# Kernel tuning notes

Measured on AMD Instinct MI355X. Metric: run time of the kernel, lower is better.

Reference implementation:

```python
import jax, jax.numpy as jnp
import numpy as np

EPS_MSG = 1e-7   # GENConv message eps
EPS_LN = 1e-5    # LayerNorm eps

N, F_IN, D, D_OUT = 32768, 64, 512, 128


def setup_inputs() -> dict:
    key = jax.random.key(0)
    ks = jax.random.split(key, 20)
    s = 0.02
    inp = {
        "batch": jax.random.normal(ks[0], (1, N, F_IN), jnp.float32),
        "W_enc": jax.random.normal(ks[1], (F_IN, D), jnp.float32) * s,
        "b_enc": jnp.zeros((D,), jnp.float32),
        "Wf": jax.random.normal(ks[2], (D, D_OUT), jnp.float32) * s,
        "bf": jnp.zeros((D_OUT,), jnp.float32),
    }
    for l in range(2):
        inp[f"t{l}"] = jnp.array(1.0, jnp.float32)           # learnable softmax temperature
        inp[f"W1_{l}"] = jax.random.normal(ks[3 + 6 * l], (D, 2 * D), jnp.float32) * s
        inp[f"b1_{l}"] = jnp.zeros((2 * D,), jnp.float32)
        inp[f"g_{l}"] = jnp.ones((2 * D,), jnp.float32)      # LN gamma
        inp[f"be_{l}"] = jnp.zeros((2 * D,), jnp.float32)    # LN beta
        inp[f"W2_{l}"] = jax.random.normal(ks[4 + 6 * l], (2 * D, D), jnp.float32) * s
        inp[f"b2_{l}"] = jnp.zeros((D,), jnp.float32)
    return inp


def _layer_norm(z, g, b):
    mu = jnp.mean(z, axis=-1, keepdims=True)
    var = jnp.var(z, axis=-1, keepdims=True)
    return (z - mu) * jax.lax.rsqrt(var + EPS_LN) * g + b


def _deepgcn_layer(x, t, W1, b1, g, be, W2, b2):
    # res+ block: h = conv(act(norm(x))); return x + h   (norm is Identity here)
    h = jax.nn.relu(x)                       # [n, d]
    # GENConv with complete graph: msg_j = relu(h_j) + eps (independent of target i)
    m = jax.nn.relu(h) + EPS_MSG             # [n, d]
    alpha = jax.nn.softmax(t * m, axis=0)    # per-channel softmax over all source nodes
    agg = jnp.sum(alpha * m, axis=0)         # [d]  -- identical for every target node
    out = h + agg[None, :]                   # + x_dst residual inside GENConv
    # GENConv MLP: Linear(d,2d) -> LayerNorm -> ReLU -> Linear(2d,d)
    z = jax.nn.relu(_layer_norm(out @ W1 + b1, g, be))
    out = z @ W2 + b2
    return x + out


def reference(batch, W_enc, b_enc, Wf, bf,
              t0, W1_0, b1_0, g_0, be_0, W2_0, b2_0,
              t1, W1_1, b1_1, g_1, be_1, W2_1, b2_1):
    bsz, n, _ = batch.shape
    x = batch.reshape(bsz * n, -1) @ W_enc + b_enc   # node encoder
    x = _deepgcn_layer(x, t0, W1_0, b1_0, g_0, be_0, W2_0, b2_0)
    x = _deepgcn_layer(x, t1, W1_1, b1_1, g_1, be_1, W2_1, b2_1)
    x = jax.nn.relu(x)                               # layers[0].act(layers[0].norm(x)), norm=Identity
    out = x @ Wf + bf
    return out.reshape(bsz, n, -1)
```

## Files before the change

### kernel.cpp

```cpp
#include <hip/hip_runtime.h>

#define DEV __device__ __forceinline__

typedef __attribute__((ext_vector_type(8))) short s8v;
typedef __attribute__((ext_vector_type(4))) float f4v;

DEV short f2bf(float f) {
  unsigned u = __builtin_bit_cast(unsigned, f);
  u += 0x7fffu + ((u >> 16) & 1u);
  return (short)(u >> 16);
}
DEV float bf2f(short s) {
  unsigned u = ((unsigned)(unsigned short)s) << 16;
  return __builtin_bit_cast(float, u);
}

DEV f4v mfma_16x16x32_bf16(s8v a, s8v b, f4v c) {
  asm("v_mfma_f32_16x16x32_bf16 %0, %1, %2, %0" : "+v"(c) : "v"(a), "v"(b));
  return c;
}

DEV s8v relu8(s8v a) {
#pragma unroll
  for (int i = 0; i < 8; ++i) a[i] = a[i] > (short)0 ? a[i] : (short)0;
  return a;
}

__global__ __launch_bounds__(256) void tconv_k(const float* __restrict__ in,
                                               short* __restrict__ out,
                                               int K, int N) {
  __shared__ float t[64][65];
  const int nb = blockIdx.x * 64, kb = blockIdx.y * 64;
  const int c = threadIdx.x & 63, r0 = threadIdx.x >> 6;
#pragma unroll
  for (int rr = 0; rr < 64; rr += 4)
    t[rr + r0][c] = in[(size_t)(kb + rr + r0) * N + nb + c];
  __syncthreads();
#pragma unroll
  for (int rr = 0; rr < 64; rr += 4)
    out[(size_t)(nb + rr + r0) * K + kb + c] = f2bf(t[c][rr + r0]);
}

__global__ __launch_bounds__(256) void conv_k(const float* __restrict__ in,
                                              short* __restrict__ out, int n4) {
  int i = blockIdx.x * 256 + threadIdx.x;
  if (i >= n4) return;
  float4 v = ((const float4*)in)[i];
  short4 o;
  o.x = f2bf(v.x);
  o.y = f2bf(v.y);
  o.z = f2bf(v.z);
  o.w = f2bf(v.w);
  ((short4*)out)[i] = o;
}

__global__ __launch_bounds__(256) void zero_k(float* p, int n) {
  int i = blockIdx.x * 256 + threadIdx.x;
  if (i < n) p[i] = 0.f;
}

__global__ __launch_bounds__(256) void finalize_k(const float* __restrict__ sums,
                                                  const float* __restrict__ W1,
                                                  const float* __restrict__ b1,
                                                  float* __restrict__ biasEff) {
  __shared__ float agg[512];
  const int tid = threadIdx.x;
  for (int d = tid; d < 512; d += 256) agg[d] = sums[512 + d] / sums[d];
  __syncthreads();
  const int j = blockIdx.x * 256 + tid;
  float a = b1[j];
  for (int d = 0; d < 512; ++d) a += agg[d] * W1[(size_t)d * 1024 + j];
  biasEff[j] = a;
}

__global__ __launch_bounds__(256) void ln_relu_k(short* __restrict__ z,
                                                 const float* __restrict__ g,
                                                 const float* __restrict__ be) {
  const int row = blockIdx.x * 4 + (threadIdx.x >> 6);
  const int lane = threadIdx.x & 63;
  short* zr = z + (size_t)row * 1024;
  s8v c0 = *(const s8v*)&zr[lane * 8];
  s8v c1 = *(const s8v*)&zr[512 + lane * 8];
  float v[16];
  float s = 0.f, q = 0.f;
#pragma unroll
  for (int i = 0; i < 8; ++i) { v[i] = bf2f(c0[i]); v[8 + i] = bf2f(c1[i]); }
#pragma unroll
  for (int i = 0; i < 16; ++i) { s += v[i]; q += v[i] * v[i]; }
#pragma unroll
  for (int o = 32; o > 0; o >>= 1) { s += __shfl_xor(s, o); q += __shfl_xor(q, o); }
  float mu = s * (1.f / 1024.f);
  float var = q * (1.f / 1024.f) - mu * mu;
  float rs = rsqrtf(var + 1e-5f);
  float gv[16], bv[16];
#pragma unroll
  for (int i = 0; i < 8; ++i) {
    gv[i] = g[lane * 8 + i];      gv[8 + i] = g[512 + lane * 8 + i];
    bv[i] = be[lane * 8 + i];     bv[8 + i] = be[512 + lane * 8 + i];
  }
  s8v o0, o1;
#pragma unroll
  for (int i = 0; i < 8; ++i) {
    o0[i] = f2bf(fmaxf((v[i] - mu) * rs * gv[i] + bv[i], 0.f));
    o1[i] = f2bf(fmaxf((v[8 + i] - mu) * rs * gv[8 + i] + bv[8 + i], 0.f));
  }
  *(s8v*)&zr[lane * 8] = o0;
  *(s8v*)&zr[512 + lane * 8] = o1;
}

#define F_ADD   1
#define F_WF32  2
#define F_WBF   4
#define F_SM    8
#define F_RELUA 16

template <int FLAGS>
__global__ __launch_bounds__(256) void gemm_k(const short* __restrict__ A,
                                              const short* __restrict__ Bt,
                                              const float* __restrict__ bias,
                                              const short* __restrict__ Xin,
                                              short* __restrict__ Cb,
                                              float* __restrict__ Cf,
                                              const float* __restrict__ tptr,
                                              float* __restrict__ sums,
                                              int M, int N, int K) {
  __shared__ short lA[128 * 32];
  __shared__ short lB[128 * 32];
  const int tid = threadIdx.x;
  const int lane = tid & 63, wid = tid >> 6;
  const int wr = wid >> 1, wc = wid & 1;
  const int nwg = gridDim.x * gridDim.y;
  const int wg = blockIdx.y * gridDim.x + blockIdx.x;
  const int swz = (wg & 7) * (nwg >> 3) + (wg >> 3);
  const int bx = swz % gridDim.x, by = swz / gridDim.x;
  const int brow = by * 128, bcol = bx * 128;
  const int l15 = lane & 15, lhi = lane >> 4;
  f4v acc[4][4] = {};

  for (int k0 = 0; k0 < K; k0 += 32) {
#pragma unroll
    for (int r = 0; r < 2; ++r) {
      int chunk = r * 256 + wid * 64 + lane;
      int row = chunk >> 2, kc = (chunk & 3) << 3;
      const short* ga = A + (size_t)(brow + row) * K + (k0 + kc);
      const short* gb = Bt + (size_t)(bcol + row) * K + (k0 + kc);
      __builtin_amdgcn_global_load_lds(
          (const __attribute__((address_space(1))) void*)ga,
          (__attribute__((address_space(3))) void*)&lA[(r * 256 + wid * 64) * 8],
          16, 0, 0);
      __builtin_amdgcn_global_load_lds(
          (const __attribute__((address_space(1))) void*)gb,
          (__attribute__((address_space(3))) void*)&lB[(r * 256 + wid * 64) * 8],
          16, 0, 0);
    }
    __syncthreads();
    s8v af[4], bfr[4];
#pragma unroll
    for (int i = 0; i < 4; ++i) {
      af[i]  = *(const s8v*)&lA[(wr * 64 + i * 16 + l15) * 32 + lhi * 8];
      bfr[i] = *(const s8v*)&lB[(wc * 64 + i * 16 + l15) * 32 + lhi * 8];
      if (FLAGS & F_RELUA) af[i] = relu8(af[i]);
    }
#pragma unroll
    for (int mi = 0; mi < 4; ++mi)
#pragma unroll
      for (int ni = 0; ni < 4; ++ni)
        acc[mi][ni] = mfma_16x16x32_bf16(af[mi], bfr[ni], acc[mi][ni]);
    __syncthreads();
  }

  const float tv = (FLAGS & F_SM) ? tptr[0] : 0.f;
  float* sred = (float*)lA;
  if (FLAGS & F_SM) {
    sred[tid] = 0.f;
    __syncthreads();
  }
#pragma unroll
  for (int ni = 0; ni < 4; ++ni) {
    int col = bcol + wc * 64 + ni * 16 + l15;
    float bv = bias[col];
    float se = 0.f, sem = 0.f;
#pragma unroll
    for (int mi = 0; mi < 4; ++mi) {
#pragma unroll
      for (int r = 0; r < 4; ++r) {
        int row = brow + wr * 64 + mi * 16 + lhi * 4 + r;
        size_t idx = (size_t)row * N + col;
        float v = acc[mi][ni][r] + bv;
        if (FLAGS & F_ADD) v += bf2f(Xin[idx]);
        if (FLAGS & F_WF32) Cf[idx] = v;
        if (FLAGS & F_WBF) Cb[idx] = f2bf(v);
        if (FLAGS & F_SM) {
          float m = fmaxf(v, 0.f) + 1e-7f;
          float e = __expf(tv * m);
          se += e;
          sem += e * m;
        }
      }
    }
    if (FLAGS & F_SM) {
      se += __shfl_xor(se, 16);   se += __shfl_xor(se, 32);
      sem += __shfl_xor(sem, 16); sem += __shfl_xor(sem, 32);
      if (lhi == 0) {
        atomicAdd(&sred[wc * 64 + ni * 16 + l15], se);
        atomicAdd(&sred[128 + wc * 64 + ni * 16 + l15], sem);
      }
    }
  }
  if (FLAGS & F_SM) {
    __syncthreads();
    int v = tid >> 7, c = tid & 127;
    atomicAdd(&sums[v * 512 + bcol + c], sred[v * 128 + c]);
  }
}

extern "C" void kernel_launch(void* const* d_in, const int* in_sizes, int n_in,
                              void* d_out, int out_size, void* d_ws,
                              size_t ws_size, hipStream_t stream) {
  (void)in_sizes; (void)n_in; (void)out_size; (void)ws_size;
  const float* batch = (const float*)d_in[0];
  const float* W_enc = (const float*)d_in[1];
  const float* b_enc = (const float*)d_in[2];
  const float* Wf    = (const float*)d_in[3];
  const float* bfv   = (const float*)d_in[4];
  const float* tptr[2] = {(const float*)d_in[5],  (const float*)d_in[12]};
  const float* W1[2]   = {(const float*)d_in[6],  (const float*)d_in[13]};
  const float* b1[2]   = {(const float*)d_in[7],  (const float*)d_in[14]};
  const float* g[2]    = {(const float*)d_in[8],  (const float*)d_in[15]};
  const float* be[2]   = {(const float*)d_in[9],  (const float*)d_in[16]};
  const float* W2[2]   = {(const float*)d_in[10], (const float*)d_in[17]};
  const float* b2[2]   = {(const float*)d_in[11], (const float*)d_in[18]};
  float* out = (float*)d_out;

  const int M = 32768;
  char* ws = (char*)d_ws;
  size_t off = 0;
  auto alloc = [&](size_t bytes) -> char* {
    char* p = ws + off;
    off += (bytes + 255) & ~(size_t)255;
    return p;
  };
  short* xbf    = (short*)alloc((size_t)M * 512 * 2);
  short* zbuf   = (short*)alloc((size_t)M * 1024 * 2);
  short* bbuf   = (short*)alloc((size_t)M * 64 * 2);
  short* wencT  = (short*)alloc(512 * 64 * 2);
  short* w1T0   = (short*)alloc(1024 * 512 * 2);
  short* w2T0   = (short*)alloc(512 * 1024 * 2);
  short* w1T1   = (short*)alloc(1024 * 512 * 2);
  short* w2T1   = (short*)alloc(512 * 1024 * 2);
  short* wfT    = (short*)alloc(128 * 512 * 2);
  float* sums   = (float*)alloc(2 * 1024 * 4);
  float* biasEff= (float*)alloc(1024 * 4);
  short* w1T[2] = {w1T0, w1T1};
  short* w2T[2] = {w2T0, w2T1};

  tconv_k<<<dim3(512 / 64, 64 / 64), 256, 0, stream>>>(W_enc, wencT, 64, 512);
  tconv_k<<<dim3(1024 / 64, 512 / 64), 256, 0, stream>>>(W1[0], w1T[0], 512, 1024);
  tconv_k<<<dim3(512 / 64, 1024 / 64), 256, 0, stream>>>(W2[0], w2T[0], 1024, 512);
  tconv_k<<<dim3(1024 / 64, 512 / 64), 256, 0, stream>>>(W1[1], w1T[1], 512, 1024);
  tconv_k<<<dim3(512 / 64, 1024 / 64), 256, 0, stream>>>(W2[1], w2T[1], 1024, 512);
  tconv_k<<<dim3(128 / 64, 512 / 64), 256, 0, stream>>>(Wf, wfT, 512, 128);

  conv_k<<<(M * 64 / 4 + 255) / 256, 256, 0, stream>>>(batch, bbuf, M * 64 / 4);
  zero_k<<<(2048 + 255) / 256, 256, 0, stream>>>(sums, 2048);

  gemm_k<F_WBF | F_SM><<<dim3(512 / 128, M / 128), 256, 0, stream>>>(
      bbuf, wencT, b_enc, nullptr, xbf, nullptr, tptr[0], sums, M, 512, 64);

  for (int l = 0; l < 2; ++l) {
    finalize_k<<<4, 256, 0, stream>>>(sums + l * 1024, W1[l], b1[l], biasEff);
    gemm_k<F_WBF | F_RELUA><<<dim3(1024 / 128, M / 128), 256, 0, stream>>>(
        xbf, w1T[l], biasEff, nullptr, zbuf, nullptr, nullptr, nullptr,
        M, 1024, 512);
    ln_relu_k<<<M / 4, 256, 0, stream>>>(zbuf, g[l], be[l]);
    if (l == 0) {
      gemm_k<F_ADD | F_WBF | F_SM><<<dim3(512 / 128, M / 128), 256, 0, stream>>>(
          zbuf, w2T[l], b2[l], xbf, xbf, nullptr, tptr[1], sums + 1024,
          M, 512, 1024);
    } else {
      gemm_k<F_ADD | F_WBF><<<dim3(512 / 128, M / 128), 256, 0, stream>>>(
          zbuf, w2T[l], b2[l], xbf, xbf, nullptr, nullptr, nullptr,
          M, 512, 1024);
    }
  }

  gemm_k<F_WF32 | F_RELUA><<<dim3(128 / 128, M / 128), 256, 0, stream>>>(
      xbf, wfT, bfv, nullptr, nullptr, out, nullptr, nullptr, M, 128, 512);
}
```

Before: 426.7 us.

## Double GEMM K-tile to 64 with XOR-swizzled LDS and parallelize finalize

The GEMM main loop now stages a 64-wide K slice per iteration instead of 32. This halves the number of barrier pairs and raises MFMA work per sync. LDS rows are 128 bytes, and the load chunks are stored with an XOR swizzle on the row index so fragment reads avoid bank conflicts. The finalize kernel is split across 64 blocks with a partial-sum reduction over 16 groups instead of 4 blocks doing 512-long serial dot products, which removes a long serial tail at small cost in LDS usage.

```diff
diff --git a/kernel.cpp b/kernel.cpp
--- a/kernel.cpp
+++ b/kernel.cpp
@@ -64,13 +64,26 @@
                                                   const float* __restrict__ b1,
                                                   float* __restrict__ biasEff) {
   __shared__ float agg[512];
+  __shared__ float part[16][16];
   const int tid = threadIdx.x;
   for (int d = tid; d < 512; d += 256) agg[d] = sums[512 + d] / sums[d];
   __syncthreads();
-  const int j = blockIdx.x * 256 + tid;
-  float a = b1[j];
-  for (int d = 0; d < 512; ++d) a += agg[d] * W1[(size_t)d * 1024 + j];
-  biasEff[j] = a;
+  const int j = blockIdx.x * 16 + (tid & 15);
+  const int grp = tid >> 4;
+  float p = 0.f;
+#pragma unroll 4
+  for (int dd = 0; dd < 32; ++dd) {
+    int d = grp * 32 + dd;
+    p += agg[d] * W1[(size_t)d * 1024 + j];
+  }
+  part[grp][tid & 15] = p;
+  __syncthreads();
+  if (tid < 16) {
+    float a = b1[blockIdx.x * 16 + tid];
+#pragma unroll
+    for (int g = 0; g < 16; ++g) a += part[g][tid];
+    biasEff[blockIdx.x * 16 + tid] = a;
+  }
 }
 
 __global__ __launch_bounds__(256) void ln_relu_k(short* __restrict__ z,
@@ -124,8 +137,8 @@
                                               const float* __restrict__ tptr,
                                               float* __restrict__ sums,
                                               int M, int N, int K) {
-  __shared__ short lA[128 * 32];
-  __shared__ short lB[128 * 32];
+  __shared__ short lA[128 * 64];
+  __shared__ short lB[128 * 64];
   const int tid = threadIdx.x;
   const int lane = tid & 63, wid = tid >> 6;
   const int wr = wid >> 1, wc = wid & 1;
@@ -137,11 +150,12 @@
   const int l15 = lane & 15, lhi = lane >> 4;
   f4v acc[4][4] = {};
 
-  for (int k0 = 0; k0 < K; k0 += 32) {
-#pragma unroll
-    for (int r = 0; r < 2; ++r) {
-      int chunk = r * 256 + wid * 64 + lane;
-      int row = chunk >> 2, kc = (chunk & 3) << 3;
+  for (int k0 = 0; k0 < K; k0 += 64) {
+#pragma unroll
+    for (int r = 0; r < 4; ++r) {
+      int chunk = r * 256 + tid;
+      int row = chunk >> 3;
+      int kc = ((chunk & 7) ^ (row & 7)) << 3;
       const short* ga = A + (size_t)(brow + row) * K + (k0 + kc);
       const short* gb = Bt + (size_t)(bcol + row) * K + (k0 + kc);
       __builtin_amdgcn_global_load_lds(
@@ -154,18 +168,25 @@
           16, 0, 0);
     }
     __syncthreads();
-    s8v af[4], bfr[4];
-#pragma unroll
-    for (int i = 0; i < 4; ++i) {
-      af[i]  = *(const s8v*)&lA[(wr * 64 + i * 16 + l15) * 32 + lhi * 8];
-      bfr[i] = *(const s8v*)&lB[(wc * 64 + i * 16 + l15) * 32 + lhi * 8];
-      if (FLAGS & F_RELUA) af[i] = relu8(af[i]);
-    }
-#pragma unroll
-    for (int mi = 0; mi < 4; ++mi)
-#pragma unroll
-      for (int ni = 0; ni < 4; ++ni)
-        acc[mi][ni] = mfma_16x16x32_bf16(af[mi], bfr[ni], acc[mi][ni]);
+#pragma unroll
+    for (int kk = 0; kk < 2; ++kk) {
+      s8v af[4], bfr[4];
+#pragma unroll
+      for (int i = 0; i < 4; ++i) {
+        const int rowA = wr * 64 + i * 16 + l15;
+        const int rowB = wc * 64 + i * 16 + l15;
+        const int cA = ((kk * 4 + lhi) ^ (rowA & 7)) << 3;
+        const int cB = ((kk * 4 + lhi) ^ (rowB & 7)) << 3;
+        af[i]  = *(const s8v*)&lA[rowA * 64 + cA];
+        bfr[i] = *(const s8v*)&lB[rowB * 64 + cB];
+        if (FLAGS & F_RELUA) af[i] = relu8(af[i]);
+      }
+#pragma unroll
+      for (int mi = 0; mi < 4; ++mi)
+#pragma unroll
+        for (int ni = 0; ni < 4; ++ni)
+          acc[mi][ni] = mfma_16x16x32_bf16(af[mi], bfr[ni], acc[mi][ni]);
+    }
     __syncthreads();
   }
 
@@ -268,7 +289,7 @@
       bbuf, wencT, b_enc, nullptr, xbf, nullptr, tptr[0], sums, M, 512, 64);
 
   for (int l = 0; l < 2; ++l) {
-    finalize_k<<<4, 256, 0, stream>>>(sums + l * 1024, W1[l], b1[l], biasEff);
+    finalize_k<<<64, 256, 0, stream>>>(sums + l * 1024, W1[l], b1[l], biasEff);
     gemm_k<F_WBF | F_RELUA><<<dim3(1024 / 128, M / 128), 256, 0, stream>>>(
         xbf, w1T[l], biasEff, nullptr, zbuf, nullptr, nullptr, nullptr,
         M, 1024, 512);
```

Result: faster. 371.6 us (-12.9%).
